# Optimization experiments

Measured on AMD Instinct MI355X. Metric: run time of the kernel, lower is better.

## Reference

```python
import jax, jax.numpy as jnp
import numpy as np

B, T, N, F, C, H, O = 4, 8, 4096, 32, 32, 64, 1
RADIUS = 50.0   # adjacency_threshold on pairwise distance
EPS = 1e-5      # batchnorm eps


def setup_inputs() -> dict:
    key = jax.random.key(0)
    ks = jax.random.split(key, 8)
    x = jax.random.normal(ks[0], (B, T, N, F), jnp.float32)
    # dist_mat from random 2D node locations in a 1000x1000 area; avg degree ~32
    loc = jax.random.uniform(ks[1], (N, 2), jnp.float32) * 1000.0
    d2 = jnp.sum((loc[:, None, :] - loc[None, :, :]) ** 2, axis=-1)  # [N,N]
    adj = (d2 < RADIUS ** 2).astype(jnp.float32)                     # includes self (d=0)
    dinv = 1.0 / jnp.sqrt(jnp.maximum(adj.sum(-1), 1.0))
    adj_norm = adj * dinv[:, None] * dinv[None, :]                   # D^-1/2 A D^-1/2
    s = 0.05
    return dict(
        x=x,
        adj_norm=adj_norm,
        bn_gamma=jnp.ones((F,), jnp.float32),
        bn_beta=jnp.zeros((F,), jnp.float32),
        W_gcn=jax.random.normal(ks[2], (F, C), jnp.float32) * s,
        b_gcn=jnp.zeros((C,), jnp.float32),
        W_ih=jax.random.normal(ks[3], (C, 3 * H), jnp.float32) * s,
        W_hh=jax.random.normal(ks[4], (H, 3 * H), jnp.float32) * s,
        b_ih=jnp.zeros((3 * H,), jnp.float32),
        b_hh=jnp.zeros((3 * H,), jnp.float32),
        W_dense=jax.random.normal(ks[5], (H, O), jnp.float32) * s,
        b_dense=jnp.zeros((O,), jnp.float32),
    )


def reference(x, adj_norm, bn_gamma, bn_beta, W_gcn, b_gcn, W_ih, W_hh, b_ih, b_hh, W_dense, b_dense):
    # BatchNorm2d over feature channel (training-mode batch stats, biased var)
    mean = x.mean(axis=(0, 1, 2))
    var = x.var(axis=(0, 1, 2))
    xn = (x - mean) * jax.lax.rsqrt(var + EPS) * bn_gamma + bn_beta  # [B,T,N,F]
    # GCN association (same math every timestep -> batch over T)
    ya = jnp.einsum('mn,btnf->btmf', adj_norm, xn)                   # neighbor aggregate
    y = jnp.einsum('btnf,fc->btnc', ya, W_gcn) + b_gcn               # [B,T,N,C]
    # precompute input-gate projections, then scan GRU cell over time
    gi = jnp.einsum('btnc,ch->btnh', y, W_ih) + b_ih                 # [B,T,N,3H]
    gi = jnp.transpose(gi, (1, 0, 2, 3))                             # [T,B,N,3H]

    def step(h, g):
        gh = h @ W_hh + b_hh
        r = jax.nn.sigmoid(g[..., :H] + gh[..., :H])
        z = jax.nn.sigmoid(g[..., H:2 * H] + gh[..., H:2 * H])
        n = jnp.tanh(g[..., 2 * H:] + r * gh[..., 2 * H:])
        h_new = (1.0 - z) * n + z * h
        return h_new, h_new

    h0 = jnp.zeros((B, N, H), x.dtype)
    _, hs = jax.lax.scan(step, h0, gi)                               # [T,B,N,H]
    out = jnp.transpose(hs, (1, 0, 2, 3)) @ W_dense + b_dense        # [B,T,N,O]
    return out
```

## Files before the change

kernel.cpp:

```cpp
#include <hip/hip_runtime.h>
#include <hip/hip_bf16.h>
#include <stdint.h>

#define B_ 4
#define T_ 8
#define N_ 4096
#define F_ 32
#define BT_ (B_*T_)
#define ROWS_ (B_*N_)
#define CAP_ 128
#define EPS_ 1e-5f
#define NELEM_ (B_*T_*N_*F_)

#define WS_BNP    0
#define WS_ROWSUM 16384
#define WS_DEG    (WS_ROWSUM + 4096)
#define WS_FRG    (WS_DEG + 4096)
#define WS_PAIR   (WS_FRG + 52*256)
#define WS_XA     (WS_PAIR + 4096*CAP_*2)

typedef float v4f __attribute__((ext_vector_type(4)));
typedef _Float16 half8 __attribute__((ext_vector_type(8)));
union HU { uint32_t u[4]; half8 v; };

__device__ inline float sigm_f(float x) {
  return __builtin_amdgcn_rcpf(1.0f + __expf(-x));
}
__device__ inline uint32_t f16pair(float a, float b) {
  union { _Float16 h; unsigned short s; } x, y;
  x.h = (_Float16)a; y.h = (_Float16)b;
  return (uint32_t)x.s | ((uint32_t)y.s << 16);
}
__device__ inline void sp2(float a0, float a1, uint32_t& hi, uint32_t& lo) {
  _Float16 h0 = (_Float16)a0, h1 = (_Float16)a1;
  float r0 = a0 - (float)h0, r1 = a1 - (float)h1;
  union { _Float16 h; unsigned short s; } u0, u1, v0, v1;
  u0.h = h0; u1.h = h1; v0.h = (_Float16)r0; v1.h = (_Float16)r1;
  hi = (uint32_t)u0.s | ((uint32_t)u1.s << 16);
  lo = (uint32_t)v0.s | ((uint32_t)v1.s << 16);
}

__global__ void __launch_bounds__(256)
k_pre(const float* __restrict__ x, const float* __restrict__ A, float* __restrict__ ws) {
  if (blockIdx.x < 2048) {
    int m0 = blockIdx.x * 2;
    __shared__ int cnt[2];
    __shared__ float wsum[4][2];
    if (threadIdx.x < 2) cnt[threadIdx.x] = 0;
    __syncthreads();
    int* deg = (int*)&ws[WS_DEG];
    float2* pair = (float2*)&ws[WS_PAIR];
    const float4* A4 = (const float4*)(A + (size_t)m0 * N_);
    float4 av4[8];
#pragma unroll
    for (int r = 0; r < 2; r++)
#pragma unroll
      for (int i = 0; i < 4; i++) av4[r * 4 + i] = A4[r * 1024 + threadIdx.x + 256 * i];
    float lsum[2] = {0.f, 0.f};
#pragma unroll
    for (int r = 0; r < 2; r++)
#pragma unroll
      for (int i = 0; i < 4; i++) {
        float av[4] = {av4[r*4+i].x, av4[r*4+i].y, av4[r*4+i].z, av4[r*4+i].w};
        int nb4 = (threadIdx.x + 256 * i) * 4;
#pragma unroll
        for (int e = 0; e < 4; e++) {
          float a = av[e];
          if (a != 0.0f) {
            int p = atomicAdd(&cnt[r], 1);
            if (p < CAP_) pair[(size_t)(m0 + r) * CAP_ + p] = make_float2(__int_as_float((nb4 + e) * F_), a);
            lsum[r] += a;
          }
        }
      }
#pragma unroll
    for (int r = 0; r < 2; r++) {
      float s = lsum[r];
#pragma unroll
      for (int off = 32; off > 0; off >>= 1) s += __shfl_xor(s, off, 64);
      if ((threadIdx.x & 63) == 0) wsum[threadIdx.x >> 6][r] = s;
    }
    __syncthreads();
#pragma unroll
    for (int r = 0; r < 2; r++) {
      int c = cnt[r];
      for (int p = c + threadIdx.x; p < 68; p += 256)
        pair[(size_t)(m0 + r) * CAP_ + p] = make_float2(__int_as_float(0), 0.0f);
    }
    if (threadIdx.x < 2) {
      int r = threadIdx.x;
      deg[m0 + r] = min(cnt[r], CAP_);
      ws[WS_ROWSUM + m0 + r] = wsum[0][r] + wsum[1][r] + wsum[2][r] + wsum[3][r];
    }
  } else {
    int bnb = blockIdx.x - 2048;
    const float4* x4 = (const float4*)x;
    int tid = bnb * 256 + threadIdx.x;
    float s[4] = {0,0,0,0}, s2[4] = {0,0,0,0};
    for (int i = tid; i < NELEM_ / 4; i += 256 * 256) {
      float4 v = x4[i];
      s[0] += v.x; s2[0] += v.x * v.x;
      s[1] += v.y; s2[1] += v.y * v.y;
      s[2] += v.z; s2[2] += v.z * v.z;
      s[3] += v.w; s2[3] += v.w * v.w;
    }
    __shared__ float ls[256][4], ls2[256][4];
#pragma unroll
    for (int r = 0; r < 4; r++) { ls[threadIdx.x][r] = s[r]; ls2[threadIdx.x][r] = s2[r]; }
    __syncthreads();
    int t = threadIdx.x;
    if (t < 32) {
      int g = t >> 2, r = t & 3;
      float a = 0.f;
      for (int q = g; q < 256; q += 8) a += ls[q][r];
      ws[WS_BNP + bnb * 64 + t] = a;
    } else if (t < 64) {
      int cch = t - 32;
      int g = cch >> 2, r = cch & 3;
      float b2 = 0.f;
      for (int q = g; q < 256; q += 8) b2 += ls2[q][r];
      ws[WS_BNP + bnb * 64 + t] = b2;
    }
  }
}

__global__ void __launch_bounds__(256)
k_fold(const float* __restrict__ gamma, const float* __restrict__ beta,
       const float* __restrict__ Wg, const float* __restrict__ bg,
       const float* __restrict__ Wih, const float* __restrict__ bih,
       const float* __restrict__ Whh, const float* __restrict__ bhh,
       float* __restrict__ ws) {
  __shared__ float fb[26144];
  __shared__ float bnp4[4][64];
  float* Wx_s  = fb;
  float* Wih_s = fb + 6144;
  float* Whh_s = fb + 12288;
  float* Wg_s  = fb + 24576;
  float* Us_s  = fb + 25600;
  float* Vs_s  = fb + 25792;
  float* bns   = fb + 25984;
  float* scale_s = fb + 26048;
  float* shift_s = fb + 26080;
  float* p_s   = fb + 26112;
  int tid = threadIdx.x;
#pragma unroll
  for (int i = tid; i < 1536; i += 256) ((float4*)Wih_s)[i] = ((const float4*)Wih)[i];
#pragma unroll
  for (int i = tid; i < 3072; i += 256) ((float4*)Whh_s)[i] = ((const float4*)Whh)[i];
  if (tid < 256) { ((float4*)Wg_s)[tid] = ((const float4*)Wg)[tid]; }
  {
    int g = tid >> 6, c = tid & 63;
    float a = 0.f;
    for (int i = 0; i < 64; i++) a += ws[WS_BNP + (size_t)(g + 4 * i) * 64 + c];
    bnp4[g][c] = a;
  }
  __syncthreads();
  if (tid < 64) bns[tid] = bnp4[0][tid] + bnp4[1][tid] + bnp4[2][tid] + bnp4[3][tid];
  __syncthreads();
  if (tid < 32) {
    float cntf = (float)(B_ * T_ * N_);
    float mean = bns[tid] / cntf;
    float var = bns[32 + tid] / cntf - mean * mean;
    float sc = gamma[tid] * rsqrtf(var + EPS_);
    scale_s[tid] = sc;
    shift_s[tid] = beta[tid] - mean * sc;
  }
  __syncthreads();
  if (tid < 32) {
    float acc = 0.f;
    for (int f = 0; f < 32; f++) acc += shift_s[f] * Wg_s[f * 32 + tid];
    p_s[tid] = acc;
  }
  __syncthreads();
  for (int e = tid; e < 32 * 192; e += 256) {
    int f = e / 192, j = e % 192;
    float acc = 0.f;
#pragma unroll
    for (int c = 0; c < 32; c++) acc += Wg_s[f * 32 + c] * Wih_s[c * 192 + j];
    Wx_s[e] = scale_s[f] * acc;
  }
  if (tid < 192) {
    float au = 0.f, av = 0.f;
#pragma unroll
    for (int c = 0; c < 32; c++) { au += p_s[c] * Wih_s[c * 192 + tid]; av += bg[c] * Wih_s[c * 192 + tid]; }
    Us_s[tid] = au; Vs_s[tid] = av + bih[tid];
  }
  __syncthreads();
  int w = tid >> 6, L = tid & 63, q = L >> 4, c = L & 15;
  uint32_t* wsu = (uint32_t*)ws;
  for (int fi = w; fi < 52; fi += 4) {
    int mt, kt;
    if (fi < 32)      { mt = fi >> 2;            kt = fi & 3; }
    else if (fi < 40) { mt = 8 + ((fi - 32) >> 1); kt = (fi & 1) ? 3 : 0; }
    else              { int r = fi - 40; mt = 12 + r / 3; kt = 1 + r % 3; }
    int cls = mt >> 2;
    int col = (cls < 2) ? mt * 16 + c : 128 + (mt & 3) * 16 + c;
#pragma unroll
    for (int d = 0; d < 4; d++) {
      float a01[2];
#pragma unroll
      for (int h2 = 0; h2 < 2; h2++) {
        int k = kt * 32 + q * 8 + 2 * d + h2;
        float v;
        if (k < 32)       v = (cls == 3) ? 0.f : Wx_s[k * 192 + col];
        else if (k < 96)  v = (cls == 2) ? 0.f : Whh_s[(k - 32) * 192 + col];
        else if (k == 96) v = (cls == 3) ? 0.f : Us_s[col];
        else if (k == 97) v = (cls < 2) ? (Vs_s[col] + bhh[col]) : (cls == 2 ? Vs_s[col] : bhh[col]);
        else              v = 0.f;
        a01[h2] = v;
      }
      wsu[WS_FRG + fi * 256 + L * 4 + d] = f16pair(a01[0], a01[1]);
    }
  }
}

#define AGG_STEP(d) { \
    float vv = pv[d]; \
    v4f t0 = pb0[d], t1 = pb1[d]; \
    float2 p = pl[row * 69 + k + 4 + d]; \
    int off = __float_as_int(p.x) + fo; \
    pv[d] = p.y; \
    pb0[d] = *(const v4f*)(xb0 + off); \
    pb1[d] = *(const v4f*)(xb1 + off); \
    acc0 += vv * t0; acc1 += vv * t1; }

__global__ void __launch_bounds__(256, 8)
k_agg(const float* __restrict__ x, float* __restrict__ ws) {
  __shared__ float2 pl[32 * 69];
  int tid = threadIdx.x;
  int chunk = blockIdx.x & 15;
  int mg = blockIdx.x >> 4;
  int row = tid >> 3, f4 = tid & 7;
  int m = mg * 32 + row;
  const int* deg = (const int*)&ws[WS_DEG];
  const float2* pair = (const float2*)&ws[WS_PAIR];
  for (int qq = tid; qq < 32 * 68; qq += 256) {
    int r = qq / 68, sl = qq - r * 68;
    pl[r * 69 + sl] = pair[(size_t)(mg * 32 + r) * CAP_ + sl];
  }
  __syncthreads();
  int d0 = deg[m];
  int dm = min(d0, 64);
  int bound = dm;
  bound = max(bound, __shfl_xor(bound, 8, 64));
  bound = max(bound, __shfl_xor(bound, 16, 64));
  bound = max(bound, __shfl_xor(bound, 32, 64));
  bound = (bound + 3) & ~3;
  int bt0 = chunk * 2;
  const float* xb0 = x + (size_t)bt0 * N_ * F_;
  const float* xb1 = xb0 + N_ * F_;
  int fo = f4 * 4;
  v4f acc0 = {0,0,0,0}, acc1 = {0,0,0,0};
  v4f pb0[4], pb1[4];
  float pv[4];
#pragma unroll
  for (int d = 0; d < 4; d++) {
    float2 p = pl[row * 69 + d];
    int off = __float_as_int(p.x) + fo;
    pv[d] = p.y;
    pb0[d] = *(const v4f*)(xb0 + off);
    pb1[d] = *(const v4f*)(xb1 + off);
  }
  for (int k = 0; k < bound; k += 4) {
    AGG_STEP(0) AGG_STEP(1) AGG_STEP(2) AGG_STEP(3)
  }
  if (d0 > 64) {
    for (int k = 64; k < d0; k++) {
      float2 p = pair[(size_t)m * CAP_ + k];
      int off = __float_as_int(p.x) + fo;
      float vv = p.y;
      acc0 += vv * *(const v4f*)(xb0 + off);
      acc1 += vv * *(const v4f*)(xb1 + off);
    }
  }
  size_t ob = (size_t)bt0 * N_ * F_ + m * F_ + fo;
  *(v4f*)(ws + WS_XA + ob) = acc0;
  *(v4f*)(ws + WS_XA + ob + (size_t)N_ * F_) = acc1;
}

#define LDA(fi) (*(const half8*)(frg + (fi)*256 + L*4))
#define DO1(mt, fi, BH, BL) { half8 af = LDA(fi); \
  acc[mt] = __builtin_amdgcn_mfma_f32_16x16x32_f16(af, BH, acc[mt], 0, 0, 0); \
  acc[mt] = __builtin_amdgcn_mfma_f32_16x16x32_f16(af, BL, acc[mt], 0, 0, 0); }

__global__ void __launch_bounds__(256, 1)
k_gru(const float* __restrict__ Wd, const float* __restrict__ bd,
      const float* __restrict__ ws, float* __restrict__ out) {
  __shared__ uint32_t frg[52 * 256];
  __shared__ uint32_t hx[4 * 1344];
  {
    const uint4* gf = (const uint4*)(ws + WS_FRG);
    uint4* sf = (uint4*)frg;
    for (int i = threadIdx.x; i < 52 * 64; i += 256) sf[i] = gf[i];
  }
  __syncthreads();
  int wid = threadIdx.x >> 6, L = threadIdx.x & 63;
  int q = L >> 4, c = L & 15;
  uint32_t* hxw = hx + wid * 1344;
  int row0 = blockIdx.x * 64 + wid * 16;
  int b = row0 >> 12;
  int nb = row0 & (N_ - 1);
  float wdv[4][4];
#pragma unroll
  for (int g = 0; g < 4; g++)
#pragma unroll
    for (int r = 0; r < 4; r++) wdv[g][r] = Wd[16 * g + 4 * q + r];
  float bdv = bd[0];
  HU b3h, b3l;
#pragma unroll
  for (int d = 0; d < 4; d++) { b3h.u[d] = 0; b3l.u[d] = 0; }
  {
    float rsv = ws[WS_ROWSUM + nb + c];
    uint32_t rhi, rlo;
    sp2(rsv, 1.0f, rhi, rlo);
    if (q == 0) { b3h.u[0] = rhi; b3l.u[0] = rlo & 0xFFFFu; }
  }
  float h[4][4];
#pragma unroll
  for (int g = 0; g < 4; g++)
#pragma unroll
    for (int r = 0; r < 4; r++) h[g][r] = 0.f;

  const float* xab = ws + WS_XA;
  size_t xo0 = ((size_t)(b * T_) * N_ + nb + c) * F_ + q * 8;
  float4 xaA = *(const float4*)(xab + xo0);
  float4 xaB = *(const float4*)(xab + xo0 + 4);

  for (int t = 0; t < T_; t++) {
    float4 nxA, nxB;
    if (t < T_ - 1) {
      size_t xo = ((size_t)(b * T_ + t + 1) * N_ + nb + c) * F_ + q * 8;
      nxA = *(const float4*)(xab + xo);
      nxB = *(const float4*)(xab + xo + 4);
    }
#pragma unroll
    for (int g = 0; g < 4; g++)
#pragma unroll
      for (int rp = 0; rp < 2; rp++) {
        uint32_t phi, plo;
        sp2(h[g][2 * rp], h[g][2 * rp + 1], phi, plo);
        int pidx = 8 * g + 2 * q + rp;
        hxw[(pidx * 2 + 0) * 21 + c] = phi;
        hxw[(pidx * 2 + 1) * 21 + c] = plo;
      }
    HU b1h, b1l, b2h, b2l;
#pragma unroll
    for (int d = 0; d < 4; d++) {
      b1h.u[d] = hxw[((4 * q + d) * 2 + 0) * 21 + c];
      b1l.u[d] = hxw[((4 * q + d) * 2 + 1) * 21 + c];
      b2h.u[d] = hxw[((16 + 4 * q + d) * 2 + 0) * 21 + c];
      b2l.u[d] = hxw[((16 + 4 * q + d) * 2 + 1) * 21 + c];
    }
    v4f acc[16];
#pragma unroll
    for (int i = 0; i < 16; i++) acc[i] = (v4f){0.f, 0.f, 0.f, 0.f};
    DO1(0,1,b1h.v,b1l.v)  DO1(1,5,b1h.v,b1l.v)  DO1(2,9,b1h.v,b1l.v)  DO1(3,13,b1h.v,b1l.v)
    DO1(4,17,b1h.v,b1l.v) DO1(5,21,b1h.v,b1l.v) DO1(6,25,b1h.v,b1l.v) DO1(7,29,b1h.v,b1l.v)
    DO1(12,40,b1h.v,b1l.v) DO1(13,43,b1h.v,b1l.v) DO1(14,46,b1h.v,b1l.v) DO1(15,49,b1h.v,b1l.v)
    DO1(0,2,b2h.v,b2l.v)  DO1(1,6,b2h.v,b2l.v)  DO1(2,10,b2h.v,b2l.v) DO1(3,14,b2h.v,b2l.v)
    DO1(4,18,b2h.v,b2l.v) DO1(5,22,b2h.v,b2l.v) DO1(6,26,b2h.v,b2l.v) DO1(7,30,b2h.v,b2l.v)
    DO1(12,41,b2h.v,b2l.v) DO1(13,44,b2h.v,b2l.v) DO1(14,47,b2h.v,b2l.v) DO1(15,50,b2h.v,b2l.v)
    DO1(0,3,b3h.v,b3l.v)  DO1(1,7,b3h.v,b3l.v)  DO1(2,11,b3h.v,b3l.v) DO1(3,15,b3h.v,b3l.v)
    DO1(4,19,b3h.v,b3l.v) DO1(5,23,b3h.v,b3l.v) DO1(6,27,b3h.v,b3l.v) DO1(7,31,b3h.v,b3l.v)
    DO1(8,33,b3h.v,b3l.v) DO1(9,35,b3h.v,b3l.v) DO1(10,37,b3h.v,b3l.v) DO1(11,39,b3h.v,b3l.v)
    DO1(12,42,b3h.v,b3l.v) DO1(13,45,b3h.v,b3l.v) DO1(14,48,b3h.v,b3l.v) DO1(15,51,b3h.v,b3l.v)
    HU b0h, b0l;
    sp2(xaA.x, xaA.y, b0h.u[0], b0l.u[0]);
    sp2(xaA.z, xaA.w, b0h.u[1], b0l.u[1]);
    sp2(xaB.x, xaB.y, b0h.u[2], b0l.u[2]);
    sp2(xaB.z, xaB.w, b0h.u[3], b0l.u[3]);
    DO1(0,0,b0h.v,b0l.v)  DO1(1,4,b0h.v,b0l.v)  DO1(2,8,b0h.v,b0l.v)  DO1(3,12,b0h.v,b0l.v)
    DO1(4,16,b0h.v,b0l.v) DO1(5,20,b0h.v,b0l.v) DO1(6,24,b0h.v,b0l.v) DO1(7,28,b0h.v,b0l.v)
    DO1(8,32,b0h.v,b0l.v) DO1(9,34,b0h.v,b0l.v) DO1(10,36,b0h.v,b0l.v) DO1(11,38,b0h.v,b0l.v)
    float o = 0.f;
#pragma unroll
    for (int g = 0; g < 4; g++)
#pragma unroll
      for (int r = 0; r < 4; r++) {
        float rr = sigm_f(acc[g][r]);
        float z  = sigm_f(acc[4 + g][r]);
        float nn = 2.0f * sigm_f(2.0f * (acc[8 + g][r] + rr * acc[12 + g][r])) - 1.0f;
        float hn = z * (h[g][r] - nn) + nn;
        h[g][r] = hn;
        o += wdv[g][r] * hn;
      }
    o += __shfl_xor(o, 16, 64);
    o += __shfl_xor(o, 32, 64);
    if (L < 16) out[(size_t)(b * T_ + t) * N_ + nb + L] = o + bdv;
    xaA = nxA; xaB = nxB;
  }
}

extern "C" void kernel_launch(void* const* d_in, const int* in_sizes, int n_in,
                              void* d_out, int out_size, void* d_ws, size_t ws_size,
                              hipStream_t stream) {
  const float* x     = (const float*)d_in[0];
  const float* adj   = (const float*)d_in[1];
  const float* gamma = (const float*)d_in[2];
  const float* beta  = (const float*)d_in[3];
  const float* Wg    = (const float*)d_in[4];
  const float* bg    = (const float*)d_in[5];
  const float* Wih   = (const float*)d_in[6];
  const float* Whh   = (const float*)d_in[7];
  const float* bih   = (const float*)d_in[8];
  const float* bhh   = (const float*)d_in[9];
  const float* Wd    = (const float*)d_in[10];
  const float* bd    = (const float*)d_in[11];
  float* ws = (float*)d_ws;
  float* out = (float*)d_out;

  k_pre<<<2048 + 256, 256, 0, stream>>>(x, adj, ws);
  k_fold<<<1, 256, 0, stream>>>(gamma, beta, Wg, bg, Wih, bih, Whh, bhh, ws);
  k_agg<<<2048, 256, 0, stream>>>(x, ws);
  k_gru<<<256, 256, 0, stream>>>(Wd, bd, ws, out);
}
```

Before: 207.0 us.

## Hoist constant bias MFMAs and pipeline next-step input projection in GRU

Precomputes the time-invariant bias contribution (rowsum-based b3 term) once before the loop and seeds accumulators with it instead of recomputing 16 MFMA pairs every timestep. The input projection for step t+1 is issued during step t into a double-buffered accumulator set, so it can overlap with the recurrent part. Step 0 skips the h-term MFMAs, since h starts at zero, and the h spill to LDS moves to the end of each step. Two accumulator sets plus the bias array raise register pressure under the one-block launch bounds.

```diff
diff --git a/kernel.cpp b/kernel.cpp
--- a/kernel.cpp
+++ b/kernel.cpp
@@ -279,9 +279,12 @@
 }
 
 #define LDA(fi) (*(const half8*)(frg + (fi)*256 + L*4))
-#define DO1(mt, fi, BH, BL) { half8 af = LDA(fi); \
-  acc[mt] = __builtin_amdgcn_mfma_f32_16x16x32_f16(af, BH, acc[mt], 0, 0, 0); \
-  acc[mt] = __builtin_amdgcn_mfma_f32_16x16x32_f16(af, BL, acc[mt], 0, 0, 0); }
+#define DO1(ACC, mt, fi, BH, BL) { half8 af = LDA(fi); \
+  ACC[mt] = __builtin_amdgcn_mfma_f32_16x16x32_f16(af, BH, ACC[mt], 0, 0, 0); \
+  ACC[mt] = __builtin_amdgcn_mfma_f32_16x16x32_f16(af, BL, ACC[mt], 0, 0, 0); }
+#define DO1B(ACC, mt, fi, BH, BL) { half8 af = LDA(fi); \
+  ACC[mt] = __builtin_amdgcn_mfma_f32_16x16x32_f16(af, BH, bias[mt], 0, 0, 0); \
+  ACC[mt] = __builtin_amdgcn_mfma_f32_16x16x32_f16(af, BL, ACC[mt], 0, 0, 0); }
 
 __global__ void __launch_bounds__(256, 1)
 k_gru(const float* __restrict__ Wd, const float* __restrict__ bd,
@@ -306,6 +309,7 @@
 #pragma unroll
     for (int r = 0; r < 4; r++) wdv[g][r] = Wd[16 * g + 4 * q + r];
   float bdv = bd[0];
+
   HU b3h, b3l;
 #pragma unroll
   for (int d = 0; d < 4; d++) { b3h.u[d] = 0; b3l.u[d] = 0; }
@@ -315,6 +319,15 @@
     sp2(rsv, 1.0f, rhi, rlo);
     if (q == 0) { b3h.u[0] = rhi; b3l.u[0] = rlo & 0xFFFFu; }
   }
+
+  v4f bias[16];
+#pragma unroll
+  for (int i = 0; i < 16; i++) bias[i] = (v4f){0.f, 0.f, 0.f, 0.f};
+  DO1(bias, 0,3,b3h.v,b3l.v)  DO1(bias, 1,7,b3h.v,b3l.v)  DO1(bias, 2,11,b3h.v,b3l.v) DO1(bias, 3,15,b3h.v,b3l.v)
+  DO1(bias, 4,19,b3h.v,b3l.v) DO1(bias, 5,23,b3h.v,b3l.v) DO1(bias, 6,27,b3h.v,b3l.v) DO1(bias, 7,31,b3h.v,b3l.v)
+  DO1(bias, 8,33,b3h.v,b3l.v) DO1(bias, 9,35,b3h.v,b3l.v) DO1(bias,10,37,b3h.v,b3l.v) DO1(bias,11,39,b3h.v,b3l.v)
+  DO1(bias,12,42,b3h.v,b3l.v) DO1(bias,13,45,b3h.v,b3l.v) DO1(bias,14,48,b3h.v,b3l.v) DO1(bias,15,51,b3h.v,b3l.v)
+
   float h[4][4];
 #pragma unroll
   for (int g = 0; g < 4; g++)
@@ -323,63 +336,66 @@
 
   const float* xab = ws + WS_XA;
   size_t xo0 = ((size_t)(b * T_) * N_ + nb + c) * F_ + q * 8;
-  float4 xaA = *(const float4*)(xab + xo0);
-  float4 xaB = *(const float4*)(xab + xo0 + 4);
-
-  for (int t = 0; t < T_; t++) {
-    float4 nxA, nxB;
-    if (t < T_ - 1) {
-      size_t xo = ((size_t)(b * T_ + t + 1) * N_ + nb + c) * F_ + q * 8;
-      nxA = *(const float4*)(xab + xo);
-      nxB = *(const float4*)(xab + xo + 4);
-    }
+  float4 x0A = *(const float4*)(xab + xo0);
+  float4 x0B = *(const float4*)(xab + xo0 + 4);
+  float4 xuA = *(const float4*)(xab + xo0 + (size_t)N_ * F_);
+  float4 xuB = *(const float4*)(xab + xo0 + (size_t)N_ * F_ + 4);
+  float4 xvA, xvB;
+
+  v4f accA[16], accB[16];
+  {
+    HU b0h, b0l;
+    sp2(x0A.x, x0A.y, b0h.u[0], b0l.u[0]);
+    sp2(x0A.z, x0A.w, b0h.u[1], b0l.u[1]);
+    sp2(x0B.x, x0B.y, b0h.u[2], b0l.u[2]);
+    sp2(x0B.z, x0B.w, b0h.u[3], b0l.u[3]);
+    DO1B(accA, 0,0,b0h.v,b0l.v)  DO1B(accA, 1,4,b0h.v,b0l.v)  DO1B(accA, 2,8,b0h.v,b0l.v)  DO1B(accA, 3,12,b0h.v,b0l.v)
+    DO1B(accA, 4,16,b0h.v,b0l.v) DO1B(accA, 5,20,b0h.v,b0l.v) DO1B(accA, 6,24,b0h.v,b0l.v) DO1B(accA, 7,28,b0h.v,b0l.v)
+    DO1B(accA, 8,32,b0h.v,b0l.v) DO1B(accA, 9,34,b0h.v,b0l.v) DO1B(accA,10,36,b0h.v,b0l.v) DO1B(accA,11,38,b0h.v,b0l.v)
+  }
+  accA[12] = bias[12]; accA[13] = bias[13]; accA[14] = bias[14]; accA[15] = bias[15];
+
+  auto STEP = [&](v4f (&CUR)[16], v4f (&NXT)[16],
+                  float4& xUA, float4& xUB, float4& xLA, float4& xLB, int t) {
+    if (t < 6) {
+      size_t xo = ((size_t)(b * T_ + t + 2) * N_ + nb + c) * F_ + q * 8;
+      xLA = *(const float4*)(xab + xo);
+      xLB = *(const float4*)(xab + xo + 4);
+    }
+    if (t > 0) {
+      HU b1h, b1l, b2h, b2l;
+#pragma unroll
+      for (int d = 0; d < 4; d++) {
+        b1h.u[d] = hxw[((4 * q + d) * 2 + 0) * 21 + c];
+        b1l.u[d] = hxw[((4 * q + d) * 2 + 1) * 21 + c];
+        b2h.u[d] = hxw[((16 + 4 * q + d) * 2 + 0) * 21 + c];
+        b2l.u[d] = hxw[((16 + 4 * q + d) * 2 + 1) * 21 + c];
+      }
+      DO1(CUR, 0,1,b1h.v,b1l.v)  DO1(CUR, 1,5,b1h.v,b1l.v)  DO1(CUR, 2,9,b1h.v,b1l.v)  DO1(CUR, 3,13,b1h.v,b1l.v)
+      DO1(CUR, 4,17,b1h.v,b1l.v) DO1(CUR, 5,21,b1h.v,b1l.v) DO1(CUR, 6,25,b1h.v,b1l.v) DO1(CUR, 7,29,b1h.v,b1l.v)
+      DO1B(CUR,12,40,b1h.v,b1l.v) DO1B(CUR,13,43,b1h.v,b1l.v) DO1B(CUR,14,46,b1h.v,b1l.v) DO1B(CUR,15,49,b1h.v,b1l.v)
+      DO1(CUR, 0,2,b2h.v,b2l.v)  DO1(CUR, 1,6,b2h.v,b2l.v)  DO1(CUR, 2,10,b2h.v,b2l.v) DO1(CUR, 3,14,b2h.v,b2l.v)
+      DO1(CUR, 4,18,b2h.v,b2l.v) DO1(CUR, 5,22,b2h.v,b2l.v) DO1(CUR, 6,26,b2h.v,b2l.v) DO1(CUR, 7,30,b2h.v,b2l.v)
+      DO1(CUR,12,41,b2h.v,b2l.v) DO1(CUR,13,44,b2h.v,b2l.v) DO1(CUR,14,47,b2h.v,b2l.v) DO1(CUR,15,50,b2h.v,b2l.v)
+    }
+    if (t < 7) {
+      HU b0h, b0l;
+      sp2(xUA.x, xUA.y, b0h.u[0], b0l.u[0]);
+      sp2(xUA.z, xUA.w, b0h.u[1], b0l.u[1]);
+      sp2(xUB.x, xUB.y, b0h.u[2], b0l.u[2]);
+      sp2(xUB.z, xUB.w, b0h.u[3], b0l.u[3]);
+      DO1B(NXT, 0,0,b0h.v,b0l.v)  DO1B(NXT, 1,4,b0h.v,b0l.v)  DO1B(NXT, 2,8,b0h.v,b0l.v)  DO1B(NXT, 3,12,b0h.v,b0l.v)
+      DO1B(NXT, 4,16,b0h.v,b0l.v) DO1B(NXT, 5,20,b0h.v,b0l.v) DO1B(NXT, 6,24,b0h.v,b0l.v) DO1B(NXT, 7,28,b0h.v,b0l.v)
+      DO1B(NXT, 8,32,b0h.v,b0l.v) DO1B(NXT, 9,34,b0h.v,b0l.v) DO1B(NXT,10,36,b0h.v,b0l.v) DO1B(NXT,11,38,b0h.v,b0l.v)
+    }
+    float o = 0.f;
 #pragma unroll
     for (int g = 0; g < 4; g++)
 #pragma unroll
-      for (int rp = 0; rp < 2; rp++) {
-        uint32_t phi, plo;
-        sp2(h[g][2 * rp], h[g][2 * rp + 1], phi, plo);
-        int pidx = 8 * g + 2 * q + rp;
-        hxw[(pidx * 2 + 0) * 21 + c] = phi;
-        hxw[(pidx * 2 + 1) * 21 + c] = plo;
-      }
-    HU b1h, b1l, b2h, b2l;
-#pragma unroll
-    for (int d = 0; d < 4; d++) {
-      b1h.u[d] = hxw[((4 * q + d) * 2 + 0) * 21 + c];
-      b1l.u[d] = hxw[((4 * q + d) * 2 + 1) * 21 + c];
-      b2h.u[d] = hxw[((16 + 4 * q + d) * 2 + 0) * 21 + c];
-      b2l.u[d] = hxw[((16 + 4 * q + d) * 2 + 1) * 21 + c];
-    }
-    v4f acc[16];
-#pragma unroll
-    for (int i = 0; i < 16; i++) acc[i] = (v4f){0.f, 0.f, 0.f, 0.f};
-    DO1(0,1,b1h.v,b1l.v)  DO1(1,5,b1h.v,b1l.v)  DO1(2,9,b1h.v,b1l.v)  DO1(3,13,b1h.v,b1l.v)
-    DO1(4,17,b1h.v,b1l.v) DO1(5,21,b1h.v,b1l.v) DO1(6,25,b1h.v,b1l.v) DO1(7,29,b1h.v,b1l.v)
-    DO1(12,40,b1h.v,b1l.v) DO1(13,43,b1h.v,b1l.v) DO1(14,46,b1h.v,b1l.v) DO1(15,49,b1h.v,b1l.v)
-    DO1(0,2,b2h.v,b2l.v)  DO1(1,6,b2h.v,b2l.v)  DO1(2,10,b2h.v,b2l.v) DO1(3,14,b2h.v,b2l.v)
-    DO1(4,18,b2h.v,b2l.v) DO1(5,22,b2h.v,b2l.v) DO1(6,26,b2h.v,b2l.v) DO1(7,30,b2h.v,b2l.v)
-    DO1(12,41,b2h.v,b2l.v) DO1(13,44,b2h.v,b2l.v) DO1(14,47,b2h.v,b2l.v) DO1(15,50,b2h.v,b2l.v)
-    DO1(0,3,b3h.v,b3l.v)  DO1(1,7,b3h.v,b3l.v)  DO1(2,11,b3h.v,b3l.v) DO1(3,15,b3h.v,b3l.v)
-    DO1(4,19,b3h.v,b3l.v) DO1(5,23,b3h.v,b3l.v) DO1(6,27,b3h.v,b3l.v) DO1(7,31,b3h.v,b3l.v)
-    DO1(8,33,b3h.v,b3l.v) DO1(9,35,b3h.v,b3l.v) DO1(10,37,b3h.v,b3l.v) DO1(11,39,b3h.v,b3l.v)
-    DO1(12,42,b3h.v,b3l.v) DO1(13,45,b3h.v,b3l.v) DO1(14,48,b3h.v,b3l.v) DO1(15,51,b3h.v,b3l.v)
-    HU b0h, b0l;
-    sp2(xaA.x, xaA.y, b0h.u[0], b0l.u[0]);
-    sp2(xaA.z, xaA.w, b0h.u[1], b0l.u[1]);
-    sp2(xaB.x, xaB.y, b0h.u[2], b0l.u[2]);
-    sp2(xaB.z, xaB.w, b0h.u[3], b0l.u[3]);
-    DO1(0,0,b0h.v,b0l.v)  DO1(1,4,b0h.v,b0l.v)  DO1(2,8,b0h.v,b0l.v)  DO1(3,12,b0h.v,b0l.v)
-    DO1(4,16,b0h.v,b0l.v) DO1(5,20,b0h.v,b0l.v) DO1(6,24,b0h.v,b0l.v) DO1(7,28,b0h.v,b0l.v)
-    DO1(8,32,b0h.v,b0l.v) DO1(9,34,b0h.v,b0l.v) DO1(10,36,b0h.v,b0l.v) DO1(11,38,b0h.v,b0l.v)
-    float o = 0.f;
-#pragma unroll
-    for (int g = 0; g < 4; g++)
-#pragma unroll
       for (int r = 0; r < 4; r++) {
-        float rr = sigm_f(acc[g][r]);
-        float z  = sigm_f(acc[4 + g][r]);
-        float nn = 2.0f * sigm_f(2.0f * (acc[8 + g][r] + rr * acc[12 + g][r])) - 1.0f;
+        float rr = sigm_f(CUR[g][r]);
+        float z  = sigm_f(CUR[4 + g][r]);
+        float nn = 2.0f * sigm_f(2.0f * (CUR[8 + g][r] + rr * CUR[12 + g][r])) - 1.0f;
         float hn = z * (h[g][r] - nn) + nn;
         h[g][r] = hn;
         o += wdv[g][r] * hn;
@@ -387,7 +403,24 @@
     o += __shfl_xor(o, 16, 64);
     o += __shfl_xor(o, 32, 64);
     if (L < 16) out[(size_t)(b * T_ + t) * N_ + nb + L] = o + bdv;
-    xaA = nxA; xaB = nxB;
+    if (t < 7) {
+#pragma unroll
+      for (int g = 0; g < 4; g++)
+#pragma unroll
+        for (int rp = 0; rp < 2; rp++) {
+          uint32_t phi, plo;
+          sp2(h[g][2 * rp], h[g][2 * rp + 1], phi, plo);
+          int pidx = 8 * g + 2 * q + rp;
+          hxw[(pidx * 2 + 0) * 21 + c] = phi;
+          hxw[(pidx * 2 + 1) * 21 + c] = plo;
+        }
+    }
+  };
+
+#pragma unroll 1
+  for (int tt = 0; tt < 4; tt++) {
+    STEP(accA, accB, xuA, xuB, xvA, xvB, 2 * tt);
+    STEP(accB, accA, xvA, xvB, xuA, xuB, 2 * tt + 1);
   }
 }
 
```

After: 203.1 us. No clear change (-1.9%).

## Split GRU hidden units across wave pairs and hoist constant bias MFMAs

Applied to the files above, without the earlier changes.

Each 16-row tile of the GRU kernel is now handled by two waves that each compute half of the hidden units, so the grid doubles to 512 blocks and per-wave MFMA and accumulator counts halve. The hidden state is exchanged through shared memory with block-wide barriers, and the output projection partial sums are combined via a small shared buffer. The bias and row-sum MFMA contributions are computed once before the time loop and reused as accumulator seeds, and the recurrent MFMAs are skipped at t=0 when h is zero. The cost is two __syncthreads per timestep and an extra shared-memory reduction for the output.

```diff
diff --git a/kernel.cpp b/kernel.cpp
--- a/kernel.cpp
+++ b/kernel.cpp
@@ -279,15 +279,19 @@
 }
 
 #define LDA(fi) (*(const half8*)(frg + (fi)*256 + L*4))
-#define DO1(mt, fi, BH, BL) { half8 af = LDA(fi); \
-  acc[mt] = __builtin_amdgcn_mfma_f32_16x16x32_f16(af, BH, acc[mt], 0, 0, 0); \
-  acc[mt] = __builtin_amdgcn_mfma_f32_16x16x32_f16(af, BL, acc[mt], 0, 0, 0); }
-
-__global__ void __launch_bounds__(256, 1)
+#define DO1(A_, fi, BH, BL) { half8 af = LDA(fi); \
+  A_ = __builtin_amdgcn_mfma_f32_16x16x32_f16(af, BH, A_, 0, 0, 0); \
+  A_ = __builtin_amdgcn_mfma_f32_16x16x32_f16(af, BL, A_, 0, 0, 0); }
+#define DO1C(A_, C_, fi, BH, BL) { half8 af = LDA(fi); \
+  A_ = __builtin_amdgcn_mfma_f32_16x16x32_f16(af, BH, C_, 0, 0, 0); \
+  A_ = __builtin_amdgcn_mfma_f32_16x16x32_f16(af, BL, A_, 0, 0, 0); }
+
+__global__ void __launch_bounds__(256, 2)
 k_gru(const float* __restrict__ Wd, const float* __restrict__ bd,
       const float* __restrict__ ws, float* __restrict__ out) {
   __shared__ uint32_t frg[52 * 256];
-  __shared__ uint32_t hx[4 * 1344];
+  __shared__ uint32_t hx[2 * 1344];
+  __shared__ float obuf[2][16];
   {
     const uint4* gf = (const uint4*)(ws + WS_FRG);
     uint4* sf = (uint4*)frg;
@@ -295,99 +299,141 @@
   }
   __syncthreads();
   int wid = threadIdx.x >> 6, L = threadIdx.x & 63;
+  int grp = wid >> 1, half = wid & 1, h2 = half * 2;
   int q = L >> 4, c = L & 15;
-  uint32_t* hxw = hx + wid * 1344;
-  int row0 = blockIdx.x * 64 + wid * 16;
-  int b = row0 >> 12;
-  int nb = row0 & (N_ - 1);
-  float wdv[4][4];
-#pragma unroll
-  for (int g = 0; g < 4; g++)
-#pragma unroll
-    for (int r = 0; r < 4; r++) wdv[g][r] = Wd[16 * g + 4 * q + r];
+  uint32_t* hxg = hx + grp * 1344;
+  int rg0 = blockIdx.x * 32 + grp * 16;
+  int b = rg0 >> 12;
+  int node0 = rg0 & (N_ - 1);
+  int fR0 = 4 * h2, fR1 = 4 * h2 + 4;
+  int fZ0 = 16 + 4 * h2, fZ1 = 20 + 4 * h2;
+  int fN0 = 32 + 2 * h2, fN1 = 34 + 2 * h2;
+  int fG0 = 40 + 3 * h2, fG1 = 43 + 3 * h2;
+  float wdv[2][4];
+#pragma unroll
+  for (int lg = 0; lg < 2; lg++)
+#pragma unroll
+    for (int r = 0; r < 4; r++) wdv[lg][r] = Wd[16 * (h2 + lg) + 4 * q + r];
   float bdv = bd[0];
+
   HU b3h, b3l;
 #pragma unroll
   for (int d = 0; d < 4; d++) { b3h.u[d] = 0; b3l.u[d] = 0; }
   {
-    float rsv = ws[WS_ROWSUM + nb + c];
+    float rsv = ws[WS_ROWSUM + node0 + c];
     uint32_t rhi, rlo;
     sp2(rsv, 1.0f, rhi, rlo);
     if (q == 0) { b3h.u[0] = rhi; b3l.u[0] = rlo & 0xFFFFu; }
   }
-  float h[4][4];
-#pragma unroll
-  for (int g = 0; g < 4; g++)
-#pragma unroll
-    for (int r = 0; r < 4; r++) h[g][r] = 0.f;
+
+  v4f bias[8];
+  {
+    v4f z4 = {0.f, 0.f, 0.f, 0.f};
+    DO1C(bias[0], z4, fR0 + 3, b3h.v, b3l.v)
+    DO1C(bias[1], z4, fR1 + 3, b3h.v, b3l.v)
+    DO1C(bias[2], z4, fZ0 + 3, b3h.v, b3l.v)
+    DO1C(bias[3], z4, fZ1 + 3, b3h.v, b3l.v)
+    DO1C(bias[4], z4, fN0 + 1, b3h.v, b3l.v)
+    DO1C(bias[5], z4, fN1 + 1, b3h.v, b3l.v)
+    DO1C(bias[6], z4, fG0 + 2, b3h.v, b3l.v)
+    DO1C(bias[7], z4, fG1 + 2, b3h.v, b3l.v)
+  }
+
+  float h[2][4];
+#pragma unroll
+  for (int lg = 0; lg < 2; lg++)
+#pragma unroll
+    for (int r = 0; r < 4; r++) h[lg][r] = 0.f;
 
   const float* xab = ws + WS_XA;
-  size_t xo0 = ((size_t)(b * T_) * N_ + nb + c) * F_ + q * 8;
-  float4 xaA = *(const float4*)(xab + xo0);
-  float4 xaB = *(const float4*)(xab + xo0 + 4);
-
+  size_t xo0 = ((size_t)(b * T_) * N_ + node0 + c) * F_ + q * 8;
+  float4 curA = *(const float4*)(xab + xo0);
+  float4 curB = *(const float4*)(xab + xo0 + 4);
+  float4 nxA, nxB;
+
+#pragma unroll 1
   for (int t = 0; t < T_; t++) {
-    float4 nxA, nxB;
+    HU b1h, b1l, b2h, b2l;
+    if (t > 0) {
+#pragma unroll
+      for (int d = 0; d < 4; d++) {
+        b1h.u[d] = hxg[((4 * q + d) * 2 + 0) * 21 + c];
+        b1l.u[d] = hxg[((4 * q + d) * 2 + 1) * 21 + c];
+        b2h.u[d] = hxg[((16 + 4 * q + d) * 2 + 0) * 21 + c];
+        b2l.u[d] = hxg[((16 + 4 * q + d) * 2 + 1) * 21 + c];
+      }
+    }
+    __syncthreads();
     if (t < T_ - 1) {
-      size_t xo = ((size_t)(b * T_ + t + 1) * N_ + nb + c) * F_ + q * 8;
+      size_t xo = ((size_t)(b * T_ + t + 1) * N_ + node0 + c) * F_ + q * 8;
       nxA = *(const float4*)(xab + xo);
       nxB = *(const float4*)(xab + xo + 4);
     }
-#pragma unroll
-    for (int g = 0; g < 4; g++)
-#pragma unroll
-      for (int rp = 0; rp < 2; rp++) {
-        uint32_t phi, plo;
-        sp2(h[g][2 * rp], h[g][2 * rp + 1], phi, plo);
-        int pidx = 8 * g + 2 * q + rp;
-        hxw[(pidx * 2 + 0) * 21 + c] = phi;
-        hxw[(pidx * 2 + 1) * 21 + c] = plo;
-      }
-    HU b1h, b1l, b2h, b2l;
-#pragma unroll
-    for (int d = 0; d < 4; d++) {
-      b1h.u[d] = hxw[((4 * q + d) * 2 + 0) * 21 + c];
-      b1l.u[d] = hxw[((4 * q + d) * 2 + 1) * 21 + c];
-      b2h.u[d] = hxw[((16 + 4 * q + d) * 2 + 0) * 21 + c];
-      b2l.u[d] = hxw[((16 + 4 * q + d) * 2 + 1) * 21 + c];
-    }
-    v4f acc[16];
-#pragma unroll
-    for (int i = 0; i < 16; i++) acc[i] = (v4f){0.f, 0.f, 0.f, 0.f};
-    DO1(0,1,b1h.v,b1l.v)  DO1(1,5,b1h.v,b1l.v)  DO1(2,9,b1h.v,b1l.v)  DO1(3,13,b1h.v,b1l.v)
-    DO1(4,17,b1h.v,b1l.v) DO1(5,21,b1h.v,b1l.v) DO1(6,25,b1h.v,b1l.v) DO1(7,29,b1h.v,b1l.v)
-    DO1(12,40,b1h.v,b1l.v) DO1(13,43,b1h.v,b1l.v) DO1(14,46,b1h.v,b1l.v) DO1(15,49,b1h.v,b1l.v)
-    DO1(0,2,b2h.v,b2l.v)  DO1(1,6,b2h.v,b2l.v)  DO1(2,10,b2h.v,b2l.v) DO1(3,14,b2h.v,b2l.v)
-    DO1(4,18,b2h.v,b2l.v) DO1(5,22,b2h.v,b2l.v) DO1(6,26,b2h.v,b2l.v) DO1(7,30,b2h.v,b2l.v)
-    DO1(12,41,b2h.v,b2l.v) DO1(13,44,b2h.v,b2l.v) DO1(14,47,b2h.v,b2l.v) DO1(15,50,b2h.v,b2l.v)
-    DO1(0,3,b3h.v,b3l.v)  DO1(1,7,b3h.v,b3l.v)  DO1(2,11,b3h.v,b3l.v) DO1(3,15,b3h.v,b3l.v)
-    DO1(4,19,b3h.v,b3l.v) DO1(5,23,b3h.v,b3l.v) DO1(6,27,b3h.v,b3l.v) DO1(7,31,b3h.v,b3l.v)
-    DO1(8,33,b3h.v,b3l.v) DO1(9,35,b3h.v,b3l.v) DO1(10,37,b3h.v,b3l.v) DO1(11,39,b3h.v,b3l.v)
-    DO1(12,42,b3h.v,b3l.v) DO1(13,45,b3h.v,b3l.v) DO1(14,48,b3h.v,b3l.v) DO1(15,51,b3h.v,b3l.v)
     HU b0h, b0l;
-    sp2(xaA.x, xaA.y, b0h.u[0], b0l.u[0]);
-    sp2(xaA.z, xaA.w, b0h.u[1], b0l.u[1]);
-    sp2(xaB.x, xaB.y, b0h.u[2], b0l.u[2]);
-    sp2(xaB.z, xaB.w, b0h.u[3], b0l.u[3]);
-    DO1(0,0,b0h.v,b0l.v)  DO1(1,4,b0h.v,b0l.v)  DO1(2,8,b0h.v,b0l.v)  DO1(3,12,b0h.v,b0l.v)
-    DO1(4,16,b0h.v,b0l.v) DO1(5,20,b0h.v,b0l.v) DO1(6,24,b0h.v,b0l.v) DO1(7,28,b0h.v,b0l.v)
-    DO1(8,32,b0h.v,b0l.v) DO1(9,34,b0h.v,b0l.v) DO1(10,36,b0h.v,b0l.v) DO1(11,38,b0h.v,b0l.v)
+    sp2(curA.x, curA.y, b0h.u[0], b0l.u[0]);
+    sp2(curA.z, curA.w, b0h.u[1], b0l.u[1]);
+    sp2(curB.x, curB.y, b0h.u[2], b0l.u[2]);
+    sp2(curB.z, curB.w, b0h.u[3], b0l.u[3]);
+    v4f acc[8];
+    if (t > 0) {
+      DO1C(acc[0], bias[0], fR0 + 1, b1h.v, b1l.v)
+      DO1C(acc[1], bias[1], fR1 + 1, b1h.v, b1l.v)
+      DO1C(acc[2], bias[2], fZ0 + 1, b1h.v, b1l.v)
+      DO1C(acc[3], bias[3], fZ1 + 1, b1h.v, b1l.v)
+      DO1C(acc[6], bias[6], fG0,     b1h.v, b1l.v)
+      DO1C(acc[7], bias[7], fG1,     b1h.v, b1l.v)
+      DO1(acc[0], fR0 + 2, b2h.v, b2l.v)
+      DO1(acc[1], fR1 + 2, b2h.v, b2l.v)
+      DO1(acc[2], fZ0 + 2, b2h.v, b2l.v)
+      DO1(acc[3], fZ1 + 2, b2h.v, b2l.v)
+      DO1(acc[6], fG0 + 1, b2h.v, b2l.v)
+      DO1(acc[7], fG1 + 1, b2h.v, b2l.v)
+      DO1(acc[0], fR0, b0h.v, b0l.v)
+      DO1(acc[1], fR1, b0h.v, b0l.v)
+      DO1(acc[2], fZ0, b0h.v, b0l.v)
+      DO1(acc[3], fZ1, b0h.v, b0l.v)
+      DO1C(acc[4], bias[4], fN0, b0h.v, b0l.v)
+      DO1C(acc[5], bias[5], fN1, b0h.v, b0l.v)
+    } else {
+      DO1C(acc[0], bias[0], fR0, b0h.v, b0l.v)
+      DO1C(acc[1], bias[1], fR1, b0h.v, b0l.v)
+      DO1C(acc[2], bias[2], fZ0, b0h.v, b0l.v)
+      DO1C(acc[3], bias[3], fZ1, b0h.v, b0l.v)
+      DO1C(acc[4], bias[4], fN0, b0h.v, b0l.v)
+      DO1C(acc[5], bias[5], fN1, b0h.v, b0l.v)
+      acc[6] = bias[6]; acc[7] = bias[7];
+    }
     float o = 0.f;
 #pragma unroll
-    for (int g = 0; g < 4; g++)
+    for (int lg = 0; lg < 2; lg++)
 #pragma unroll
       for (int r = 0; r < 4; r++) {
-        float rr = sigm_f(acc[g][r]);
-        float z  = sigm_f(acc[4 + g][r]);
-        float nn = 2.0f * sigm_f(2.0f * (acc[8 + g][r] + rr * acc[12 + g][r])) - 1.0f;
-        float hn = z * (h[g][r] - nn) + nn;
-        h[g][r] = hn;
-        o += wdv[g][r] * hn;
+        float rr = sigm_f(acc[lg][r]);
+        float zz = sigm_f(acc[2 + lg][r]);
+        float nn = 2.0f * sigm_f(2.0f * (acc[4 + lg][r] + rr * acc[6 + lg][r])) - 1.0f;
+        float hn = zz * (h[lg][r] - nn) + nn;
+        h[lg][r] = hn;
+        o += wdv[lg][r] * hn;
       }
     o += __shfl_xor(o, 16, 64);
     o += __shfl_xor(o, 32, 64);
-    if (L < 16) out[(size_t)(b * T_ + t) * N_ + nb + L] = o + bdv;
-    xaA = nxA; xaB = nxB;
+    if (half == 1 && L < 16) obuf[grp][L] = o;
+    if (t < T_ - 1) {
+#pragma unroll
+      for (int lg = 0; lg < 2; lg++)
+#pragma unroll
+        for (int rp = 0; rp < 2; rp++) {
+          uint32_t phi, plo;
+          sp2(h[lg][2 * rp], h[lg][2 * rp + 1], phi, plo);
+          int pidx = 8 * (h2 + lg) + 2 * q + rp;
+          hxg[(pidx * 2 + 0) * 21 + c] = phi;
+          hxg[(pidx * 2 + 1) * 21 + c] = plo;
+        }
+    }
+    __syncthreads();
+    if (half == 0 && L < 16)
+      out[(size_t)(b * T_ + t) * N_ + node0 + L] = o + obuf[grp][L] + bdv;
+    curA = nxA; curB = nxB;
   }
 }
 
@@ -412,5 +458,5 @@
   k_pre<<<2048 + 256, 256, 0, stream>>>(x, adj, ws);
   k_fold<<<1, 256, 0, stream>>>(gamma, beta, Wg, bg, Wih, bih, Whh, bhh, ws);
   k_agg<<<2048, 256, 0, stream>>>(x, ws);
-  k_gru<<<256, 256, 0, stream>>>(Wd, bd, ws, out);
-}
+  k_gru<<<512, 256, 0, stream>>>(Wd, bd, ws, out);
+}
```

Result: no change. 203.4 us (-1.7%).
